# Kernel tuning notes

Hardware: AMD Instinct MI355X
Metric: run time of the kernel (lower is better)

Reference implementation:

```python
import jax, jax.numpy as jnp
from jax import lax
import numpy as np

B, T, D_IN, H, EPS = 32, 256, 256, 1024, 1e-5


def setup_inputs() -> dict:
    key = jax.random.key(0)
    ks = jax.random.split(key, 9)
    s = lambda fan_in: 1.0 / np.sqrt(fan_in)
    merged0, merged1 = D_IN + H, H + H
    series = jax.random.normal(ks[0], (B, T, D_IN), dtype=jnp.float32)
    # Fused gate weights: columns are [in_gate | forget | candidate | out] (4 Linears concatenated)
    W0 = jax.random.uniform(ks[1], (merged0, 4 * H), jnp.float32, -s(merged0), s(merged0))
    b0 = jax.random.uniform(ks[2], (4 * H,), jnp.float32, -s(merged0), s(merged0))
    g0 = jnp.ones((H,), jnp.float32)
    beta0 = jnp.zeros((H,), jnp.float32)
    W1 = jax.random.uniform(ks[3], (merged1, 4 * H), jnp.float32, -s(merged1), s(merged1))
    b1 = jax.random.uniform(ks[4], (4 * H,), jnp.float32, -s(merged1), s(merged1))
    g1 = jnp.ones((H,), jnp.float32)
    beta1 = jnp.zeros((H,), jnp.float32)
    return {"series": series, "W0": W0, "b0": b0, "g0": g0, "beta0": beta0,
            "W1": W1, "b1": b1, "g1": g1, "beta1": beta1}


def _layer_norm(x, g, beta):
    mu = jnp.mean(x, axis=-1, keepdims=True)
    var = jnp.mean((x - mu) ** 2, axis=-1, keepdims=True)
    return (x - mu) * lax.rsqrt(var + EPS) * g + beta


def _run_layer(x_seq, W, b, g, beta):
    # x_seq: [B, T, D]; exp-gated LSTM cell scanned over time
    batch = x_seq.shape[0]

    def step(carry, x_t):
        h, c = carry
        merged = jnp.concatenate([x_t, h], axis=-1)          # [B, D+H]
        z = merged @ W + b                                    # [B, 4H] fused 4 projections
        zi, zf, zc, zo = jnp.split(z, 4, axis=-1)
        in_gate = jnp.exp(jnp.clip(zi, -6.0, 3.0))
        forget_gate = jnp.exp(jnp.clip(zf, -6.0, 3.0))
        candidate = jnp.tanh(zc)
        c_next = forget_gate * c + in_gate * candidate
        h_next = jax.nn.sigmoid(zo) * jnp.tanh(_layer_norm(c_next, g, beta))
        return (h_next, c_next), h_next

    h0 = jnp.zeros((batch, H), x_seq.dtype)
    c0 = jnp.zeros((batch, H), x_seq.dtype)
    _, hs = lax.scan(step, (h0, c0), jnp.swapaxes(x_seq, 0, 1))  # hs: [T, B, H]
    return jnp.swapaxes(hs, 0, 1)


def reference(series, W0, b0, g0, beta0, W1, b1, g1, beta1):
    out = _run_layer(series, W0, b0, g0, beta0)
    # dropout p=0.0 -> identity between layers
    out = _run_layer(out, W1, b1, g1, beta1)
    return out[:, -1, :]
```

## Files before the change

### kernel.cpp

```cpp
#include <hip/hip_runtime.h>
#include <hip/hip_bf16.h>
#include <cstddef>

typedef __bf16 bf16_t;
typedef bf16_t bf16x8 __attribute__((ext_vector_type(8)));
typedef bf16_t bf16x4 __attribute__((ext_vector_type(4)));
typedef float  f32x4  __attribute__((ext_vector_type(4)));
typedef unsigned u32x4 __attribute__((ext_vector_type(4)));
typedef unsigned u32x2 __attribute__((ext_vector_type(2)));

#define T_STEPS 256
#define BATCH   32
#define HDIM    1024
#define ZDIM    4096

constexpr size_t SZ_HSEQ  = (size_t)8192 * 1024 * 2;
constexpr size_t SZ_HBUF  = (size_t)2 * 32 * 1024 * 4;
constexpr size_t SZ_SP    = (size_t)2 * 4 * 8 * 128 * 4;
constexpr size_t SZ_HST   = (size_t)32 * 1024 * 2;
constexpr size_t SZ_CST   = (size_t)32 * 1024 * 4;
constexpr size_t SZ_MU    = 256;
constexpr size_t SZ_TAIL  = SZ_HBUF + SZ_SP + 2*SZ_HST + SZ_CST + SZ_MU;
constexpr int    FILL_WORDS = (int)((SZ_HBUF + SZ_SP) / 4);

constexpr int SLAB_STRIDE = 264;
constexpr int HL_STRIDE   = 1040;
constexpr int SCAN_LDS    = 2 * 64 * SLAB_STRIDE * 2;

__global__ void init_fill(unsigned* __restrict__ p, int n) {
    int i = blockIdx.x * blockDim.x + threadIdx.x;
    if (i < n) p[i] = 0xFFFFFFFFu;
}

__device__ __forceinline__ void split_bf16(float v, bf16_t& hi, bf16_t& lo) {
    hi = (bf16_t)v;
    lo = (bf16_t)(v - (float)hi);
}
__device__ __forceinline__ unsigned short bf16_bits(bf16_t f) {
    union { unsigned short u; bf16_t f2; } x; x.f2 = f; return x.u;
}
__device__ __forceinline__ float tanh_fast(float x) {
    float e = __expf(2.f * x);
    return 1.f - 2.f * __builtin_amdgcn_rcpf(e + 1.f);
}
__device__ __forceinline__ void bar_lds() {
    asm volatile("s_waitcnt lgkmcnt(0)" ::: "memory");
    __builtin_amdgcn_s_barrier();
    asm volatile("" ::: "memory");
}

template<int KTOT, int MODE>
__global__ __launch_bounds__(256) void gemm_xp(
    const float*  __restrict__ Afp,
    const bf16_t* __restrict__ Ahi,
    const bf16_t* __restrict__ Alo,
    const float*  __restrict__ W,
    const float*  __restrict__ bias,
    float*        __restrict__ xp,
    int t0)
{
    __shared__ bf16_t Ash[64][40], Asl[64][40], Bsh[64][40], Bsl[64][40];
    const int bm = blockIdx.x / (ZDIM/64);
    const int bn = blockIdx.x % (ZDIM/64);
    const int tid  = threadIdx.x;
    const int lane = tid & 63;
    const int w    = tid >> 6;
    const int wm = w >> 1, wn = w & 1;
    const int q   = lane >> 4;
    const int l15 = lane & 15;

    f32x4 acc[2][2] = {};

    const int sm = tid & 63;
    const int sk = (tid >> 6) * 8;
    const int gr = t0*32 + bm*64 + sm;
    const float*  Arow  = nullptr;
    const bf16_t* Ahrow = nullptr;
    const bf16_t* Alrow = nullptr;
    if constexpr (MODE == 0) {
        int tt = gr >> 5, bb = gr & 31;
        Arow = Afp + ((size_t)bb * T_STEPS + tt) * 256;
    } else {
        Ahrow = Ahi + (size_t)gr * HDIM;
        Alrow = Alo + (size_t)gr * HDIM;
    }
    const int gcol = bn*64 + sm;

    for (int k0 = 0; k0 < KTOT; k0 += 32) {
        if constexpr (MODE == 0) {
            f32x4 a0 = *(const f32x4*)(Arow + k0 + sk);
            f32x4 a1 = *(const f32x4*)(Arow + k0 + sk + 4);
            #pragma unroll
            for (int j = 0; j < 4; ++j) {
                split_bf16(a0[j], Ash[sm][sk+j],   Asl[sm][sk+j]);
                split_bf16(a1[j], Ash[sm][sk+4+j], Asl[sm][sk+4+j]);
            }
        } else {
            *(bf16x8*)&Ash[sm][sk] = *(const bf16x8*)(Ahrow + k0 + sk);
            *(bf16x8*)&Asl[sm][sk] = *(const bf16x8*)(Alrow + k0 + sk);
        }
        #pragma unroll
        for (int j = 0; j < 8; ++j) {
            float wv = W[(size_t)(k0 + sk + j) * ZDIM + gcol];
            split_bf16(wv, Bsh[sm][sk+j], Bsl[sm][sk+j]);
        }
        __syncthreads();
        #pragma unroll
        for (int mt = 0; mt < 2; ++mt) {
            #pragma unroll
            for (int nt = 0; nt < 2; ++nt) {
                bf16x8 ah = *(const bf16x8*)&Ash[wm*32 + mt*16 + l15][q*8];
                bf16x8 al = *(const bf16x8*)&Asl[wm*32 + mt*16 + l15][q*8];
                bf16x8 bh = *(const bf16x8*)&Bsh[wn*32 + nt*16 + l15][q*8];
                bf16x8 bl = *(const bf16x8*)&Bsl[wn*32 + nt*16 + l15][q*8];
                acc[mt][nt] = __builtin_amdgcn_mfma_f32_16x16x32_bf16(ah, bh, acc[mt][nt], 0, 0, 0);
                acc[mt][nt] = __builtin_amdgcn_mfma_f32_16x16x32_bf16(al, bh, acc[mt][nt], 0, 0, 0);
                acc[mt][nt] = __builtin_amdgcn_mfma_f32_16x16x32_bf16(ah, bl, acc[mt][nt], 0, 0, 0);
            }
        }
        __syncthreads();
    }
    #pragma unroll
    for (int mt = 0; mt < 2; ++mt) {
        int row = bm*64 + wm*32 + mt*16 + q*4;
        #pragma unroll
        for (int nt = 0; nt < 2; ++nt) {
            int col = bn*64 + wn*32 + nt*16 + l15;
            float bia = bias[col];
            #pragma unroll
            for (int r = 0; r < 4; ++r)
                xp[(size_t)(row + r)*ZDIM + col] = acc[mt][nt][r] + bia;
        }
    }
}

__global__ __launch_bounds__(256, 1) void scan_kernel(
    const float* __restrict__ Wh,
    const float* __restrict__ xp,
    const float* __restrict__ gamma,
    const float* __restrict__ beta,
    unsigned*    Hbuf,
    unsigned*    Sp,
    bf16_t*      __restrict__ hseq_hi,
    bf16_t*      __restrict__ hseq_lo,
    float*       __restrict__ outlast,
    bf16_t*      __restrict__ hst_hi,
    bf16_t*      __restrict__ hst_lo,
    float*       __restrict__ cstate,
    float*       __restrict__ mustate,
    int t0, int t1)
{
    extern __shared__ char smem[];
    bf16_t* slab_hi = (bf16_t*)smem;
    bf16_t* slab_lo = (bf16_t*)(smem + 64*SLAB_STRIDE*2);
    bf16_t* hl_hi   = (bf16_t*)smem;
    bf16_t* hl_lo   = (bf16_t*)(smem + 8*HL_STRIDE*2);
    float*  swred   = (float*)(smem + 16*HL_STRIDE*2);
    float*  sredS   = swred + 64;

    const int gid = blockIdx.x >> 6;
    const int lid = blockIdx.x & 63;
    const int B0  = gid * 8;
    const int H0  = lid * 16;
    const int tid  = threadIdx.x;
    const int lane = tid & 63;
    const int w    = tid >> 6;
    const int q    = lane >> 4;
    const int l15  = lane & 15;

    bf16x8 wf_hi[32], wf_lo[32];
    {
        const int kw   = tid >> 6;
        const int strip= (tid >> 4) & 3;
        const int col  = tid & 15;
        const int gc2  = strip*1024 + H0 + col;
        const int rr_w = col*4 + strip;
        #pragma unroll
        for (int s = 0; s < 4; ++s) {
            for (int j = 0; j < 64; ++j) {
                int kk = j*4 + kw;
                float v = Wh[(size_t)(s*256 + kk)*ZDIM + gc2];
                bf16_t hi, lo; split_bf16(v, hi, lo);
                slab_hi[rr_w*SLAB_STRIDE + kk] = hi;
                slab_lo[rr_w*SLAB_STRIDE + kk] = lo;
            }
            __syncthreads();
            #pragma unroll
            for (int kbl = 0; kbl < 8; ++kbl) {
                wf_hi[s*8+kbl] = *(const bf16x8*)&slab_hi[(16*w + l15)*SLAB_STRIDE + kbl*32 + q*8];
                wf_lo[s*8+kbl] = *(const bf16x8*)&slab_lo[(16*w + l15)*SLAB_STRIDE + kbl*32 + q*8];
            }
            __syncthreads();
        }
    }

    const int  bidx  = l15;
    const bool valid = bidx < 8;
    const int  batch = B0 + bidx;
    const int  hcl   = 4*w + q;
    const int  hcg   = H0 + hcl;
    const size_t xpbase = (size_t)batch * ZDIM + (size_t)H0 + hcl;
    const int hrow  = (l15 < 8) ? l15 : 7;

    const int cb = tid * 4;

    float g_own = 0.f, b_own = 0.f;
    if (valid) { g_own = gamma[hcg]; b_own = beta[hcg]; }

    float c = 0.f, mu_own = 0.f;
    if (t0 > 0) {
        if (valid) {
            c = cstate[(size_t)batch*HDIM + hcg];
            mu_own = mustate[batch];
        }
        #pragma unroll
        for (int r = 0; r < 8; ++r) {
            *(bf16x4*)&hl_hi[r*HL_STRIDE + cb] = *(const bf16x4*)&hst_hi[(size_t)(B0+r)*HDIM + cb];
            *(bf16x4*)&hl_lo[r*HL_STRIDE + cb] = *(const bf16x4*)&hst_lo[(size_t)(B0+r)*HDIM + cb];
        }
    }
    __syncthreads();

    float xpv[4] = {0.f, 0.f, 0.f, 0.f};
    if (valid) {
        const float* xpt = xp + xpbase;
        #pragma unroll
        for (int r = 0; r < 4; ++r) xpv[r] = xpt[(size_t)r * 1024];
    }

    const bool is_l0 = (hseq_hi != nullptr);

    #pragma unroll 1
    for (int t = t0; t < t1; ++t) {
        f32x4 acc_hh = {0.f,0.f,0.f,0.f}, acc_lh = acc_hh, acc_hl = acc_hh;
        if (t > 0) {
            const bf16_t* Bh = hl_hi + (size_t)hrow * HL_STRIDE + q*8;
            const bf16_t* Bl = hl_lo + (size_t)hrow * HL_STRIDE + q*8;
            #pragma unroll
            for (int kb = 0; kb < 32; ++kb) {
                bf16x8 bh = *(const bf16x8*)(Bh + kb*32);
                bf16x8 bv = *(const bf16x8*)(Bl + kb*32);
                acc_hh = __builtin_amdgcn_mfma_f32_16x16x32_bf16(wf_hi[kb], bh, acc_hh, 0, 0, 0);
                acc_lh = __builtin_amdgcn_mfma_f32_16x16x32_bf16(wf_lo[kb], bh, acc_lh, 0, 0, 0);
                acc_hl = __builtin_amdgcn_mfma_f32_16x16x32_bf16(wf_hi[kb], bv, acc_hl, 0, 0, 0);
            }
        }
        float z[4];
        #pragma unroll
        for (int r = 0; r < 4; ++r)
            z[r] = ((acc_lh[r] + acc_hl[r]) + acc_hh[r]) + xpv[r];

        if (valid && t+1 < t1) {
            const float* xpt = xp + (size_t)(t+1 - t0) * (BATCH*ZDIM) + xpbase;
            #pragma unroll
            for (int r = 0; r < 4; ++r) xpv[r] = xpt[(size_t)r * 1024];
        }

        float zi = fminf(fmaxf(z[0], -6.f), 3.f);
        float zf = fminf(fmaxf(z[1], -6.f), 3.f);
        float ig = __expf(zi);
        float fg = __expf(zf);
        float cand = tanh_fast(z[2]);
        float sg = 1.f / (1.f + __expf(-z[3]));
        c = fg * c + ig * cand;

        const int par = t & 1;
        const unsigned tg = (unsigned)(t & 3);

        float dm = valid ? (c - mu_own) : 0.f;
        float s1 = dm, s2 = dm*dm;
        s1 += __shfl_xor(s1, 16); s2 += __shfl_xor(s2, 16);
        s1 += __shfl_xor(s1, 32); s2 += __shfl_xor(s2, 32);
        if (lane < 8) { swred[(w*8+lane)*2] = s1; swred[(w*8+lane)*2+1] = s2; }
        bar_lds();

        if (tid < 8) {
            float S1p = swred[tid*2]     + swred[(8+tid)*2]
                      + swred[(16+tid)*2]+ swred[(24+tid)*2];
            float S2p = swred[tid*2+1]     + swred[(8+tid)*2+1]
                      + swred[(16+tid)*2+1]+ swred[(24+tid)*2+1];
            u32x2 pk;
            pk[0] = (__float_as_uint(S1p) & ~3u) | tg;
            pk[1] = (__float_as_uint(S2p) & ~3u) | tg;
            *(volatile u32x2*)(Sp + (((size_t)par*4 + gid)*8 + tid)*128 + (size_t)lid*2) = pk;
        }

        {
            const int rr = tid >> 5, jj = tid & 31;
            volatile const u32x4* spb =
                (volatile const u32x4*)(Sp + (((size_t)par*4 + gid)*8 + rr)*128 + (size_t)jj*4);
            u32x4 sv = *spb;
            while ((((sv[0]^tg)|(sv[1]^tg)|(sv[2]^tg)|(sv[3]^tg)) & 3u) != 0u) sv = *spb;
            float s1p = __uint_as_float(sv[0] & ~3u) + __uint_as_float(sv[2] & ~3u);
            float s2p = __uint_as_float(sv[1] & ~3u) + __uint_as_float(sv[3] & ~3u);
            #pragma unroll
            for (int m = 1; m < 32; m <<= 1) {
                s1p += __shfl_xor(s1p, m);
                s2p += __shfl_xor(s2p, m);
            }
            if (jj == 0) { sredS[rr*2] = s1p; sredS[rr*2+1] = s2p; }
        }
        bar_lds();

        const bool carry = (t == t1-1) && (t1 < T_STEPS);
        if (valid) {
            float S1 = sredS[bidx*2], S2 = sredS[bidx*2+1];
            float dmu = S1 * (1.f/1024.f);
            float mu  = mu_own + dmu;
            float var = S2 * (1.f/1024.f) - dmu*dmu;
            float rsig = rsqrtf(var + 1e-5f);
            mu_own = mu;
            float ln  = (c - mu) * rsig * g_own + b_own;
            float hval = sg * tanh_fast(ln);
            bf16_t hhi, hlo; split_bf16(hval, hhi, hlo);
            unsigned pk = ((unsigned)bf16_bits(hhi) << 16)
                        | ((unsigned)bf16_bits(hlo) & 0xFFFCu) | tg;
            *(volatile unsigned*)(Hbuf + ((size_t)par*32 + batch)*HDIM + hcg) = pk;
            if (is_l0) {
                hseq_hi[((size_t)t*32 + batch)*HDIM + hcg] = hhi;
                hseq_lo[((size_t)t*32 + batch)*HDIM + hcg] = hlo;
            }
            if (carry) {
                hst_hi[(size_t)batch*HDIM + hcg] = hhi;
                hst_lo[(size_t)batch*HDIM + hcg] = hlo;
            }
            if (outlast && t == T_STEPS-1)
                outlast[(size_t)batch*HDIM + hcg] = hval;
        }

        if (t + 1 < t1) {
            volatile const u32x4* hb0 =
                (volatile const u32x4*)(Hbuf + ((size_t)par*32 + B0)*HDIM + cb);
            u32x4 hv[8];
            #pragma unroll
            for (int r = 0; r < 8; ++r) hv[r] = hb0[(size_t)r*(HDIM/4)];
            bool all_ok = false;
            while (!all_ok) {
                all_ok = true;
                #pragma unroll
                for (int r = 0; r < 8; ++r) {
                    if ((((hv[r][0]^tg)|(hv[r][1]^tg)|(hv[r][2]^tg)|(hv[r][3]^tg)) & 3u) != 0u) {
                        hv[r] = hb0[(size_t)r*(HDIM/4)];
                        all_ok = false;
                    }
                }
            }
            #pragma unroll
            for (int r = 0; r < 8; ++r) {
                unsigned d0 = (hv[r][0] >> 16)    | (hv[r][1] & 0xFFFF0000u);
                unsigned d1 = (hv[r][2] >> 16)    | (hv[r][3] & 0xFFFF0000u);
                unsigned e0 = (hv[r][0] & 0xFFFFu)| (hv[r][1] << 16);
                unsigned e1 = (hv[r][2] & 0xFFFFu)| (hv[r][3] << 16);
                u32x2 dh; dh[0] = d0; dh[1] = d1;
                u32x2 dl; dl[0] = e0; dl[1] = e1;
                *(u32x2*)&hl_hi[r*HL_STRIDE + cb] = dh;
                *(u32x2*)&hl_lo[r*HL_STRIDE + cb] = dl;
            }
            bar_lds();
        }
    }

    if (t1 < T_STEPS) {
        if (valid) cstate[(size_t)batch*HDIM + hcg] = c;
        if (lid == 0 && w == 0 && q == 0 && valid) mustate[batch] = mu_own;
    }
}

extern "C" void kernel_launch(void* const* d_in, const int* in_sizes, int n_in,
                              void* d_out, int out_size, void* d_ws, size_t ws_size,
                              hipStream_t stream) {
    (void)in_sizes; (void)n_in;
    const float* series = (const float*)d_in[0];
    const float* W0  = (const float*)d_in[1];
    const float* b0  = (const float*)d_in[2];
    const float* g0  = (const float*)d_in[3];
    const float* be0 = (const float*)d_in[4];
    const float* W1  = (const float*)d_in[5];
    const float* b1  = (const float*)d_in[6];
    const float* g1  = (const float*)d_in[7];
    const float* be1 = (const float*)d_in[8];
    float* out = (float*)d_out;
    unsigned char* ws = (unsigned char*)d_ws;

    int cT = 0;
    const int cands[4] = {256, 128, 64, 32};
    for (int i = 0; i < 4; ++i) {
        size_t need = (size_t)cands[i]*32*ZDIM*4 + 2*SZ_HSEQ + SZ_TAIL;
        if (need <= ws_size) { cT = cands[i]; break; }
    }
    if (cT == 0) {
        (void)hipMemsetAsync(d_out, 0, (size_t)out_size * sizeof(float), stream);
        return;
    }
    const size_t sz_xp = (size_t)cT*32*ZDIM*4;
    unsigned char* p = ws;
    float*    xp      = (float*)p;    p += sz_xp;
    bf16_t*   hseq_hi = (bf16_t*)p;   p += SZ_HSEQ;
    bf16_t*   hseq_lo = (bf16_t*)p;   p += SZ_HSEQ;
    unsigned* Hbuf    = (unsigned*)p; p += SZ_HBUF;
    unsigned* Sp      = (unsigned*)p; p += SZ_SP;
    bf16_t*   hst_hi  = (bf16_t*)p;   p += SZ_HST;
    bf16_t*   hst_lo  = (bf16_t*)p;   p += SZ_HST;
    float*    cstate  = (float*)p;    p += SZ_CST;
    float*    mustate = (float*)p;

    (void)hipFuncSetAttribute((const void*)scan_kernel,
                              hipFuncAttributeMaxDynamicSharedMemorySize, SCAN_LDS);

    init_fill<<<(FILL_WORDS + 255)/256, 256, 0, stream>>>(Hbuf, FILL_WORDS);

    const int nch = T_STEPS / cT;
    const int gemm_grid = (cT*32/64) * (ZDIM/64);

    for (int ci = 0; ci < nch; ++ci) {
        int t0 = ci*cT, t1 = t0 + cT;
        gemm_xp<256, 0><<<gemm_grid, 256, 0, stream>>>(
            series, nullptr, nullptr, W0, b0, xp, t0);
        scan_kernel<<<256, 256, SCAN_LDS, stream>>>(
            W0 + (size_t)256*ZDIM, xp, g0, be0, Hbuf, Sp,
            hseq_hi, hseq_lo, nullptr, hst_hi, hst_lo, cstate, mustate, t0, t1);
    }
    for (int ci = 0; ci < nch; ++ci) {
        int t0 = ci*cT, t1 = t0 + cT;
        gemm_xp<1024, 1><<<gemm_grid, 256, 0, stream>>>(
            nullptr, hseq_hi, hseq_lo, W1, b1, xp, t0);
        scan_kernel<<<256, 256, SCAN_LDS, stream>>>(
            W1 + (size_t)1024*ZDIM, xp, g1, be1, Hbuf, Sp,
            nullptr, nullptr, out, hst_hi, hst_lo, cstate, mustate, t0, t1);
    }
}
```

Measured before the change: 4.996 ms.

## Exchange hidden state as single fp16 with packed flags, drop lo-h MFMA

Hidden state is now exchanged between blocks as one fp16 value per element, packed two per 32-bit word with a one-bit step tag in each half, instead of a bf16 hi/lo pair per word. This halves the inter-block exchange buffer and the spin-poll traffic, and the recurrent matmul drops from three MFMAs per k-block to two (fp16 hi and scaled-lo weights times fp16 h). The flag pattern changes to a 2-bit tag split across the two halves. The change also adds s_sleep to the spin loops, moves the next-step xp prefetch after the partial-sum publish, and re-initialises the buffer before layer 1. The risk is lower precision in h, since fp16 has an 11-bit mantissa whose lowest bit is used for the tag, compared with the bf16 hi/lo pair.

```diff
diff --git a/kernel.cpp b/kernel.cpp
--- a/kernel.cpp
+++ b/kernel.cpp
@@ -3,8 +3,10 @@
 #include <cstddef>
 
 typedef __bf16 bf16_t;
+typedef _Float16 f16_t;
 typedef bf16_t bf16x8 __attribute__((ext_vector_type(8)));
 typedef bf16_t bf16x4 __attribute__((ext_vector_type(4)));
+typedef f16_t  f16x8  __attribute__((ext_vector_type(8)));
 typedef float  f32x4  __attribute__((ext_vector_type(4)));
 typedef unsigned u32x4 __attribute__((ext_vector_type(4)));
 typedef unsigned u32x2 __attribute__((ext_vector_type(2)));
@@ -15,7 +17,7 @@
 #define ZDIM    4096
 
 constexpr size_t SZ_HSEQ  = (size_t)8192 * 1024 * 2;
-constexpr size_t SZ_HBUF  = (size_t)2 * 32 * 1024 * 4;
+constexpr size_t SZ_HBUF  = (size_t)2 * 32 * 512 * 4;
 constexpr size_t SZ_SP    = (size_t)2 * 4 * 8 * 128 * 4;
 constexpr size_t SZ_HST   = (size_t)32 * 1024 * 2;
 constexpr size_t SZ_CST   = (size_t)32 * 1024 * 4;
@@ -36,8 +38,8 @@
     hi = (bf16_t)v;
     lo = (bf16_t)(v - (float)hi);
 }
-__device__ __forceinline__ unsigned short bf16_bits(bf16_t f) {
-    union { unsigned short u; bf16_t f2; } x; x.f2 = f; return x.u;
+__device__ __forceinline__ unsigned short f16_bits(f16_t f) {
+    union { unsigned short u; f16_t f2; } x; x.f2 = f; return x.u;
 }
 __device__ __forceinline__ float tanh_fast(float x) {
     float e = __expf(2.f * x);
@@ -151,12 +153,11 @@
     int t0, int t1)
 {
     extern __shared__ char smem[];
-    bf16_t* slab_hi = (bf16_t*)smem;
-    bf16_t* slab_lo = (bf16_t*)(smem + 64*SLAB_STRIDE*2);
-    bf16_t* hl_hi   = (bf16_t*)smem;
-    bf16_t* hl_lo   = (bf16_t*)(smem + 8*HL_STRIDE*2);
-    float*  swred   = (float*)(smem + 16*HL_STRIDE*2);
-    float*  sredS   = swred + 64;
+    f16_t* slab_hi = (f16_t*)smem;
+    f16_t* slab_lo = (f16_t*)(smem + 64*SLAB_STRIDE*2);
+    f16_t* hl      = (f16_t*)smem;
+    float* swred   = (float*)(smem + 8*HL_STRIDE*2);
+    float* sredS   = swred + 64;
 
     const int gid = blockIdx.x >> 6;
     const int lid = blockIdx.x & 63;
@@ -168,7 +169,7 @@
     const int q    = lane >> 4;
     const int l15  = lane & 15;
 
-    bf16x8 wf_hi[32], wf_lo[32];
+    f16x8 wf_hi[32], wf_lo[32];
     {
         const int kw   = tid >> 6;
         const int strip= (tid >> 4) & 3;
@@ -180,15 +181,16 @@
             for (int j = 0; j < 64; ++j) {
                 int kk = j*4 + kw;
                 float v = Wh[(size_t)(s*256 + kk)*ZDIM + gc2];
-                bf16_t hi, lo; split_bf16(v, hi, lo);
+                f16_t hi = (f16_t)v;
+                f16_t lo = (f16_t)((v - (float)hi) * 2048.f);
                 slab_hi[rr_w*SLAB_STRIDE + kk] = hi;
                 slab_lo[rr_w*SLAB_STRIDE + kk] = lo;
             }
             __syncthreads();
             #pragma unroll
             for (int kbl = 0; kbl < 8; ++kbl) {
-                wf_hi[s*8+kbl] = *(const bf16x8*)&slab_hi[(16*w + l15)*SLAB_STRIDE + kbl*32 + q*8];
-                wf_lo[s*8+kbl] = *(const bf16x8*)&slab_lo[(16*w + l15)*SLAB_STRIDE + kbl*32 + q*8];
+                wf_hi[s*8+kbl] = *(const f16x8*)&slab_hi[(16*w + l15)*SLAB_STRIDE + kbl*32 + q*8];
+                wf_lo[s*8+kbl] = *(const f16x8*)&slab_lo[(16*w + l15)*SLAB_STRIDE + kbl*32 + q*8];
             }
             __syncthreads();
         }
@@ -202,7 +204,10 @@
     const size_t xpbase = (size_t)batch * ZDIM + (size_t)H0 + hcl;
     const int hrow  = (l15 < 8) ? l15 : 7;
 
-    const int cb = tid * 4;
+    const int half   = lane >> 5;
+    const int lane32 = lane & 31;
+    const int rr     = 2*w + half;
+    const int rbatch = B0 + rr;
 
     float g_own = 0.f, b_own = 0.f;
     if (valid) { g_own = gamma[hcg]; b_own = beta[hcg]; }
@@ -213,10 +218,14 @@
             c = cstate[(size_t)batch*HDIM + hcg];
             mu_own = mustate[batch];
         }
+        const int cb = tid * 4;
         #pragma unroll
         for (int r = 0; r < 8; ++r) {
-            *(bf16x4*)&hl_hi[r*HL_STRIDE + cb] = *(const bf16x4*)&hst_hi[(size_t)(B0+r)*HDIM + cb];
-            *(bf16x4*)&hl_lo[r*HL_STRIDE + cb] = *(const bf16x4*)&hst_lo[(size_t)(B0+r)*HDIM + cb];
+            bf16x4 vh = *(const bf16x4*)&hst_hi[(size_t)(B0+r)*HDIM + cb];
+            bf16x4 vl = *(const bf16x4*)&hst_lo[(size_t)(B0+r)*HDIM + cb];
+            #pragma unroll
+            for (int e = 0; e < 4; ++e)
+                hl[r*HL_STRIDE + cb + e] = (f16_t)((float)vh[e] + (float)vl[e]);
         }
     }
     __syncthreads();
@@ -232,29 +241,20 @@
 
     #pragma unroll 1
     for (int t = t0; t < t1; ++t) {
-        f32x4 acc_hh = {0.f,0.f,0.f,0.f}, acc_lh = acc_hh, acc_hl = acc_hh;
+        f32x4 acc_hh = {0.f,0.f,0.f,0.f}, acc_lh = acc_hh;
         if (t > 0) {
-            const bf16_t* Bh = hl_hi + (size_t)hrow * HL_STRIDE + q*8;
-            const bf16_t* Bl = hl_lo + (size_t)hrow * HL_STRIDE + q*8;
+            const f16_t* Bp = hl + (size_t)hrow * HL_STRIDE + q*8;
             #pragma unroll
             for (int kb = 0; kb < 32; ++kb) {
-                bf16x8 bh = *(const bf16x8*)(Bh + kb*32);
-                bf16x8 bv = *(const bf16x8*)(Bl + kb*32);
-                acc_hh = __builtin_amdgcn_mfma_f32_16x16x32_bf16(wf_hi[kb], bh, acc_hh, 0, 0, 0);
-                acc_lh = __builtin_amdgcn_mfma_f32_16x16x32_bf16(wf_lo[kb], bh, acc_lh, 0, 0, 0);
-                acc_hl = __builtin_amdgcn_mfma_f32_16x16x32_bf16(wf_hi[kb], bv, acc_hl, 0, 0, 0);
+                f16x8 b = *(const f16x8*)(Bp + kb*32);
+                acc_hh = __builtin_amdgcn_mfma_f32_16x16x32_f16(wf_hi[kb], b, acc_hh, 0, 0, 0);
+                acc_lh = __builtin_amdgcn_mfma_f32_16x16x32_f16(wf_lo[kb], b, acc_lh, 0, 0, 0);
             }
         }
         float z[4];
         #pragma unroll
         for (int r = 0; r < 4; ++r)
-            z[r] = ((acc_lh[r] + acc_hl[r]) + acc_hh[r]) + xpv[r];
-
-        if (valid && t+1 < t1) {
-            const float* xpt = xp + (size_t)(t+1 - t0) * (BATCH*ZDIM) + xpbase;
-            #pragma unroll
-            for (int r = 0; r < 4; ++r) xpv[r] = xpt[(size_t)r * 1024];
-        }
+            z[r] = (acc_hh[r] + acc_lh[r]*(1.f/2048.f)) + xpv[r];
 
         float zi = fminf(fmaxf(z[0], -6.f), 3.f);
         float zf = fminf(fmaxf(z[1], -6.f), 3.f);
@@ -266,6 +266,7 @@
 
         const int par = t & 1;
         const unsigned tg = (unsigned)(t & 3);
+        const unsigned tgpat = (unsigned)(t & 1) | (((unsigned)(t >> 1) & 1u) << 16);
 
         float dm = valid ? (c - mu_own) : 0.f;
         float s1 = dm, s2 = dm*dm;
@@ -275,8 +276,8 @@
         bar_lds();
 
         if (tid < 8) {
-            float S1p = swred[tid*2]     + swred[(8+tid)*2]
-                      + swred[(16+tid)*2]+ swred[(24+tid)*2];
+            float S1p = swred[tid*2]       + swred[(8+tid)*2]
+                      + swred[(16+tid)*2]  + swred[(24+tid)*2];
             float S2p = swred[tid*2+1]     + swred[(8+tid)*2+1]
                       + swred[(16+tid)*2+1]+ swred[(24+tid)*2+1];
             u32x2 pk;
@@ -285,12 +286,21 @@
             *(volatile u32x2*)(Sp + (((size_t)par*4 + gid)*8 + tid)*128 + (size_t)lid*2) = pk;
         }
 
+        if (valid && t+1 < t1) {
+            const float* xpt = xp + (size_t)(t+1 - t0) * (BATCH*ZDIM) + xpbase;
+            #pragma unroll
+            for (int r = 0; r < 4; ++r) xpv[r] = xpt[(size_t)r * 1024];
+        }
+
         {
-            const int rr = tid >> 5, jj = tid & 31;
+            const int prr = tid >> 5, jj = tid & 31;
             volatile const u32x4* spb =
-                (volatile const u32x4*)(Sp + (((size_t)par*4 + gid)*8 + rr)*128 + (size_t)jj*4);
+                (volatile const u32x4*)(Sp + (((size_t)par*4 + gid)*8 + prr)*128 + (size_t)jj*4);
             u32x4 sv = *spb;
-            while ((((sv[0]^tg)|(sv[1]^tg)|(sv[2]^tg)|(sv[3]^tg)) & 3u) != 0u) sv = *spb;
+            while ((((sv[0]^tg)|(sv[1]^tg)|(sv[2]^tg)|(sv[3]^tg)) & 3u) != 0u) {
+                __builtin_amdgcn_s_sleep(1);
+                sv = *spb;
+            }
             float s1p = __uint_as_float(sv[0] & ~3u) + __uint_as_float(sv[2] & ~3u);
             float s2p = __uint_as_float(sv[1] & ~3u) + __uint_as_float(sv[3] & ~3u);
             #pragma unroll
@@ -298,11 +308,12 @@
                 s1p += __shfl_xor(s1p, m);
                 s2p += __shfl_xor(s2p, m);
             }
-            if (jj == 0) { sredS[rr*2] = s1p; sredS[rr*2+1] = s2p; }
+            if (jj == 0) { sredS[prr*2] = s1p; sredS[prr*2+1] = s2p; }
         }
         bar_lds();
 
         const bool carry = (t == t1-1) && (t1 < T_STEPS);
+        unsigned hbs = 0;
         if (valid) {
             float S1 = sredS[bidx*2], S2 = sredS[bidx*2+1];
             float dmu = S1 * (1.f/1024.f);
@@ -310,54 +321,51 @@
             float var = S2 * (1.f/1024.f) - dmu*dmu;
             float rsig = rsqrtf(var + 1e-5f);
             mu_own = mu;
-            float ln  = (c - mu) * rsig * g_own + b_own;
+            float ln   = (c - mu) * rsig * g_own + b_own;
             float hval = sg * tanh_fast(ln);
-            bf16_t hhi, hlo; split_bf16(hval, hhi, hlo);
-            unsigned pk = ((unsigned)bf16_bits(hhi) << 16)
-                        | ((unsigned)bf16_bits(hlo) & 0xFFFCu) | tg;
-            *(volatile unsigned*)(Hbuf + ((size_t)par*32 + batch)*HDIM + hcg) = pk;
             if (is_l0) {
-                hseq_hi[((size_t)t*32 + batch)*HDIM + hcg] = hhi;
-                hseq_lo[((size_t)t*32 + batch)*HDIM + hcg] = hlo;
+                bf16_t hi, lo; split_bf16(hval, hi, lo);
+                hseq_hi[((size_t)t*32 + batch)*HDIM + hcg] = hi;
+                hseq_lo[((size_t)t*32 + batch)*HDIM + hcg] = lo;
             }
             if (carry) {
-                hst_hi[(size_t)batch*HDIM + hcg] = hhi;
-                hst_lo[(size_t)batch*HDIM + hcg] = hlo;
+                bf16_t hi, lo; split_bf16(hval, hi, lo);
+                hst_hi[(size_t)batch*HDIM + hcg] = hi;
+                hst_lo[(size_t)batch*HDIM + hcg] = lo;
             }
             if (outlast && t == T_STEPS-1)
                 outlast[(size_t)batch*HDIM + hcg] = hval;
-        }
-
-        if (t + 1 < t1) {
-            volatile const u32x4* hb0 =
-                (volatile const u32x4*)(Hbuf + ((size_t)par*32 + B0)*HDIM + cb);
-            u32x4 hv[8];
-            #pragma unroll
-            for (int r = 0; r < 8; ++r) hv[r] = hb0[(size_t)r*(HDIM/4)];
-            bool all_ok = false;
-            while (!all_ok) {
-                all_ok = true;
-                #pragma unroll
-                for (int r = 0; r < 8; ++r) {
-                    if ((((hv[r][0]^tg)|(hv[r][1]^tg)|(hv[r][2]^tg)|(hv[r][3]^tg)) & 3u) != 0u) {
-                        hv[r] = hb0[(size_t)r*(HDIM/4)];
-                        all_ok = false;
-                    }
-                }
-            }
-            #pragma unroll
-            for (int r = 0; r < 8; ++r) {
-                unsigned d0 = (hv[r][0] >> 16)    | (hv[r][1] & 0xFFFF0000u);
-                unsigned d1 = (hv[r][2] >> 16)    | (hv[r][3] & 0xFFFF0000u);
-                unsigned e0 = (hv[r][0] & 0xFFFFu)| (hv[r][1] << 16);
-                unsigned e1 = (hv[r][2] & 0xFFFFu)| (hv[r][3] << 16);
-                u32x2 dh; dh[0] = d0; dh[1] = d1;
-                u32x2 dl; dl[0] = e0; dl[1] = e1;
-                *(u32x2*)&hl_hi[r*HL_STRIDE + cb] = dh;
-                *(u32x2*)&hl_lo[r*HL_STRIDE + cb] = dl;
-            }
-            bar_lds();
-        }
+            unsigned tb = (q & 1) ? ((unsigned)(t >> 1) & 1u) : ((unsigned)t & 1u);
+            hbs = ((unsigned)f16_bits((f16_t)hval) & 0xFFFEu) | tb;
+        }
+        unsigned pb2 = __shfl_xor(hbs, 16);
+        if (valid && !(q & 1)) {
+            unsigned dw = hbs | (pb2 << 16);
+            *(volatile unsigned*)(Hbuf + ((size_t)par*32 + batch)*512 + ((unsigned)hcg >> 1)) = dw;
+        }
+
+        volatile const u32x4* hb4 =
+            (volatile const u32x4*)(Hbuf + ((size_t)par*32 + rbatch)*512) + lane32;
+        u32x4 pv[4];
+        #pragma unroll
+        for (int k = 0; k < 4; ++k) pv[k] = hb4[(size_t)k*32];
+        for (;;) {
+            bool bad = false;
+            #pragma unroll
+            for (int k = 0; k < 4; ++k) {
+                unsigned m = ((pv[k][0]^tgpat)|(pv[k][1]^tgpat)
+                             |(pv[k][2]^tgpat)|(pv[k][3]^tgpat)) & 0x00010001u;
+                if (m) { pv[k] = hb4[(size_t)k*32]; bad = true; }
+            }
+            if (!bad) break;
+            __builtin_amdgcn_s_sleep(1);
+        }
+        #pragma unroll
+        for (int k = 0; k < 4; ++k) {
+            u32x4 vv = pv[k] & 0xFFFEFFFEu;
+            *(u32x4*)&hl[(size_t)rr*HL_STRIDE + (size_t)k*256 + (size_t)lane32*8] = vv;
+        }
+        bar_lds();
     }
 
     if (t1 < T_STEPS) {
@@ -407,11 +415,10 @@
     (void)hipFuncSetAttribute((const void*)scan_kernel,
                               hipFuncAttributeMaxDynamicSharedMemorySize, SCAN_LDS);
 
-    init_fill<<<(FILL_WORDS + 255)/256, 256, 0, stream>>>(Hbuf, FILL_WORDS);
-
     const int nch = T_STEPS / cT;
     const int gemm_grid = (cT*32/64) * (ZDIM/64);
 
+    init_fill<<<(FILL_WORDS + 255)/256, 256, 0, stream>>>(Hbuf, FILL_WORDS);
     for (int ci = 0; ci < nch; ++ci) {
         int t0 = ci*cT, t1 = t0 + cT;
         gemm_xp<256, 0><<<gemm_grid, 256, 0, stream>>>(
@@ -420,6 +427,7 @@
             W0 + (size_t)256*ZDIM, xp, g0, be0, Hbuf, Sp,
             hseq_hi, hseq_lo, nullptr, hst_hi, hst_lo, cstate, mustate, t0, t1);
     }
+    init_fill<<<(FILL_WORDS + 255)/256, 256, 0, stream>>>(Hbuf, FILL_WORDS);
     for (int ci = 0; ci < nch; ++ci) {
         int t0 = ci*cT, t1 = t0 + cT;
         gemm_xp<1024, 1><<<gemm_grid, 256, 0, stream>>>(
```

Measured after the change: 4.172 ms. 1.2x faster.
